# Kernel tuning notes

Measured on AMD Instinct MI355X. Metric: run time of the kernel, lower is better.

The kernel has to match this reference:

```python
import jax, jax.numpy as jnp
import numpy as np

B, P, NB = 16, 10000, 10


def setup_inputs() -> dict:
    key = jax.random.key(0)
    k1, k2, k3, k4 = jax.random.split(key, 4)
    geofeature = jax.random.normal(k1, (B, P, 9), dtype=jnp.float32)
    # neighbor indices into padded T; 0 is the zero-padding row
    nb = jax.random.randint(k2, (P, NB), 0, P + 1)
    reconmatrix = jax.random.normal(k3, (P, P), dtype=jnp.float32) / np.float32(np.sqrt(P))
    vdiff = jax.random.normal(k4, (P, NB, 3), dtype=jnp.float32)
    return {"geofeature": geofeature, "nb": nb, "reconmatrix": reconmatrix, "vdiff": vdiff}


def _ftoT(f):
    # f: [B, P, 9]. First 3 = log-rotation, last 6 = symmetric scale/shear.
    logr = f[..., :3]
    x, y, z = logr[..., 0], logr[..., 1], logr[..., 2]
    theta = jnp.sqrt(jnp.sum(logr * logr, axis=-1))  # [B, P]
    zero = jnp.zeros_like(x)
    # matches torch gather [6,0,1,3,6,2,4,5,6] over [x,y,z,-x,-y,-z,0]:
    # [[0, x, y], [-x, 0, z], [-y, -z, 0]]
    K = jnp.stack([zero, x, y, -x, zero, z, -y, -z, zero], axis=-1)
    K = K.reshape(f.shape[0], f.shape[1], 3, 3)
    cond = theta == 0
    safe_theta = jnp.where(cond, jnp.ones_like(theta), theta)
    Kn = K / safe_theta[..., None, None]
    st = jnp.sin(safe_theta)[..., None, None]
    ct = jnp.cos(safe_theta)[..., None, None]
    I = jnp.eye(3, dtype=f.dtype)
    R_rod = I + Kn * st + jnp.matmul(Kn, Kn) * (1.0 - ct)
    R = jnp.where(cond[..., None, None], I, R_rod)
    # S symmetric from features 3..8 via gather pattern [3,4,5,4,6,7,5,7,8]
    s3, s4, s5, s6, s7, s8 = (f[..., i] for i in range(3, 9))
    S = jnp.stack([s3, s4, s5, s4, s6, s7, s5, s7, s8], axis=-1)
    S = S.reshape(f.shape[0], f.shape[1], 3, 3)
    return jnp.matmul(R, S)  # [B, P, 3, 3]


def reference(geofeature, nb, reconmatrix, vdiff):
    T = _ftoT(geofeature)  # [B, P, 3, 3]
    padded = jnp.concatenate([jnp.zeros((T.shape[0], 1, 3, 3), T.dtype), T], axis=1)
    nb_T = padded[:, nb]                    # [B, P, NB, 3, 3] neighbor gather
    sum_T = nb_T + T[:, :, None]            # [B, P, NB, 3, 3]
    bdiff = jnp.einsum('bpnde,pne->bpnd', sum_T, vdiff)  # [B, P, NB, 3]
    bvec = jnp.sum(bdiff, axis=2)           # [B, P, 3]
    v = jnp.einsum('vp,bpe->bve', reconmatrix, bvec)     # [B, P, 3]
    return v
```

## Files before the change

### kernel.cpp

```cpp
#include <hip/hip_runtime.h>
#include <math.h>

#define B_    16
#define P_    10000
#define NB_   10
#define KBTOT 313
#define KBPAD 328
#define NSMAX 16

typedef __attribute__((ext_vector_type(8))) short bf16x8;
typedef __attribute__((ext_vector_type(4))) float f32x4;

static __device__ __forceinline__ unsigned short f2bf(float f) {
    unsigned u = __float_as_uint(f);
    u += 0x7fffu + ((u >> 16) & 1u);
    return (unsigned short)(u >> 16);
}

__global__ __launch_bounds__(256) void ftoT_kernel(const float* __restrict__ f,
                                                   float* __restrict__ Tm2) {
    int t = blockIdx.x * blockDim.x + threadIdx.x;
    if (t >= B_ * P_) return;
    int p = t >> 4, b = t & 15;
    const float* fp = f + ((size_t)b * P_ + p) * 9;
    float x = fp[0], y = fp[1], z = fp[2];
    float s3 = fp[3], s4 = fp[4], s5 = fp[5], s6 = fp[6], s7 = fp[7], s8 = fp[8];
    float th2 = x * x + y * y + z * z;
    float R00, R01, R02, R10, R11, R12, R20, R21, R22;
    if (th2 == 0.0f) {
        R00 = 1; R01 = 0; R02 = 0; R10 = 0; R11 = 1; R12 = 0; R20 = 0; R21 = 0; R22 = 1;
    } else {
        float theta = sqrtf(th2);
        float inv = 1.0f / theta;
        float kx = x * inv, ky = y * inv, kz = z * inv;
        float st = sinf(theta);
        float omc = 1.0f - cosf(theta);
        R00 = 1.0f - omc * (kx * kx + ky * ky);
        R01 = kx * st - omc * (ky * kz);
        R02 = ky * st + omc * (kx * kz);
        R10 = -kx * st - omc * (ky * kz);
        R11 = 1.0f - omc * (kx * kx + kz * kz);
        R12 = kz * st - omc * (kx * ky);
        R20 = -ky * st + omc * (kx * kz);
        R21 = -kz * st - omc * (kx * ky);
        R22 = 1.0f - omc * (ky * ky + kz * kz);
    }
    float* o = Tm2 + (size_t)t * 12;
    o[0] = R00 * s3 + R01 * s4 + R02 * s5;
    o[1] = R00 * s4 + R01 * s6 + R02 * s7;
    o[2] = R00 * s5 + R01 * s7 + R02 * s8;
    o[3] = R10 * s3 + R11 * s4 + R12 * s5;
    o[4] = R10 * s4 + R11 * s6 + R12 * s7;
    o[5] = R10 * s5 + R11 * s7 + R12 * s8;
    o[6] = R20 * s3 + R21 * s4 + R22 * s5;
    o[7] = R20 * s4 + R21 * s6 + R22 * s7;
    o[8] = R20 * s5 + R21 * s7 + R22 * s8;
    o[9] = 0.0f; o[10] = 0.0f; o[11] = 0.0f;
}

__global__ __launch_bounds__(256) void bvec_kernel(const float* __restrict__ Tm2,
                                                   const int* __restrict__ nb,
                                                   const float* __restrict__ vdiff,
                                                   unsigned short* __restrict__ Bf) {
    int tid = threadIdx.x;
    int bl = tid & 15, pl = tid >> 4;
    int p = blockIdx.x * 16 + pl;
    if (p >= P_) return;

    const float4* Tow = (const float4*)(Tm2 + ((size_t)p * 16 + bl) * 12);
    float4 o0 = Tow[0], o1 = Tow[1], o2 = Tow[2];

    float a0 = 0, a1 = 0, a2 = 0, vs0 = 0, vs1 = 0, vs2 = 0;
#pragma unroll
    for (int n = 0; n < NB_; n++) {
        int idx = nb[p * NB_ + n];
        const float* vd = vdiff + ((size_t)p * NB_ + n) * 3;
        float v0 = vd[0], v1 = vd[1], v2 = vd[2];
        vs0 += v0; vs1 += v1; vs2 += v2;
        if (idx > 0) {
            const float4* Tp = (const float4*)(Tm2 + ((size_t)(idx - 1) * 16 + bl) * 12);
            float4 q0 = Tp[0], q1 = Tp[1], q2 = Tp[2];
            a0 += q0.x * v0 + q0.y * v1 + q0.z * v2;
            a1 += q0.w * v0 + q1.x * v1 + q1.y * v2;
            a2 += q1.z * v0 + q1.w * v1 + q2.x * v2;
        }
    }
    a0 += o0.x * vs0 + o0.y * vs1 + o0.z * vs2;
    a1 += o0.w * vs0 + o1.x * vs1 + o1.y * vs2;
    a2 += o1.z * vs0 + o1.w * vs1 + o2.x * vs2;

    int kb = p >> 5, ii = p & 7, quad = (p >> 3) & 3;
    float vals[3] = {a0, a1, a2};
#pragma unroll
    for (int d = 0; d < 3; d++) {
        int j = bl * 3 + d;
        int t = j >> 4;
        int ln = quad * 16 + (j & 15);
        Bf[(((size_t)kb * 3 + t) * 64 + ln) * 8 + ii] = f2bf(vals[d]);
    }
}

static __device__ __forceinline__ void slot_load(const float* __restrict__ ap,
                                                 const bf16x8* __restrict__ Bv,
                                                 int l, int kb,
                                                 float4& a0, float4& a1,
                                                 bf16x8& b0, bf16x8& b1, bf16x8& b2) {
    const float4* p = (const float4*)(ap + (size_t)kb * 32);
    a0 = p[0]; a1 = p[1];
    size_t bo = (size_t)kb * 192 + l;
    b0 = Bv[bo]; b1 = Bv[bo + 64]; b2 = Bv[bo + 128];
}

static __device__ __forceinline__ void slot_mfma(const float4& a0, const float4& a1,
                                                 const bf16x8& b0, const bf16x8& b1,
                                                 const bf16x8& b2,
                                                 f32x4& acc0, f32x4& acc1, f32x4& acc2) {
    bf16x8 a;
    a[0] = (short)f2bf(a0.x); a[1] = (short)f2bf(a0.y);
    a[2] = (short)f2bf(a0.z); a[3] = (short)f2bf(a0.w);
    a[4] = (short)f2bf(a1.x); a[5] = (short)f2bf(a1.y);
    a[6] = (short)f2bf(a1.z); a[7] = (short)f2bf(a1.w);
    acc0 = __builtin_amdgcn_mfma_f32_16x16x32_bf16(a, b0, acc0, 0, 0, 0);
    acc1 = __builtin_amdgcn_mfma_f32_16x16x32_bf16(a, b1, acc1, 0, 0, 0);
    acc2 = __builtin_amdgcn_mfma_f32_16x16x32_bf16(a, b2, acc2, 0, 0, 0);
}

__global__ __launch_bounds__(256, 4) void gemm_mfma(const float* __restrict__ recon,
                                                    const unsigned short* __restrict__ Bf,
                                                    float* __restrict__ part, int KBC) {
    int l = threadIdx.x & 63;
    int w = threadIdx.x >> 6;
    int r0 = (blockIdx.x * 4 + w) * 16;
    if (r0 >= P_) return;
    int y = blockIdx.y;
    int kb0 = y * KBC;
    int kbend = kb0 + KBC; if (kbend > 320) kbend = 320;
    int kbf = kbend < 312 ? kbend : 312;
    if (kbf < kb0) kbf = kb0;
    int n = l & 15, quad = l >> 4;
    const float* ap = recon + (size_t)(r0 + n) * P_ + quad * 8;
    const bf16x8* Bv = (const bf16x8*)Bf;

    f32x4 acc0 = {0, 0, 0, 0}, acc1 = {0, 0, 0, 0}, acc2 = {0, 0, 0, 0};

    int nfull = kbf - kb0;
    if (nfull >= 2) {
        float4 s0a0, s0a1, s1a0, s1a1;
        bf16x8 s0b0, s0b1, s0b2, s1b0, s1b1, s1b2;
        slot_load(ap, Bv, l, kb0,     s0a0, s0a1, s0b0, s0b1, s0b2);
        slot_load(ap, Bv, l, kb0 + 1, s1a0, s1a1, s1b0, s1b1, s1b2);
        for (int kb = kb0 + 2; kb + 1 < kbf; kb += 2) {
            slot_mfma(s0a0, s0a1, s0b0, s0b1, s0b2, acc0, acc1, acc2);
            slot_load(ap, Bv, l, kb,     s0a0, s0a1, s0b0, s0b1, s0b2);
            slot_mfma(s1a0, s1a1, s1b0, s1b1, s1b2, acc0, acc1, acc2);
            slot_load(ap, Bv, l, kb + 1, s1a0, s1a1, s1b0, s1b1, s1b2);
        }
        slot_mfma(s0a0, s0a1, s0b0, s0b1, s0b2, acc0, acc1, acc2);
        slot_mfma(s1a0, s1a1, s1b0, s1b1, s1b2, acc0, acc1, acc2);
    }

    for (int kb = kbf; kb < kbend; ++kb) {
        int k = kb * 32 + quad * 8;
        bf16x8 a;
        if (k < P_) {
            const float4* apk = (const float4*)(recon + (size_t)(r0 + n) * P_ + k);
            float4 x0 = apk[0], x1 = apk[1];
            a[0] = (short)f2bf(x0.x); a[1] = (short)f2bf(x0.y);
            a[2] = (short)f2bf(x0.z); a[3] = (short)f2bf(x0.w);
            a[4] = (short)f2bf(x1.x); a[5] = (short)f2bf(x1.y);
            a[6] = (short)f2bf(x1.z); a[7] = (short)f2bf(x1.w);
        } else {
            a = (bf16x8)0;
        }
        size_t bo = (size_t)kb * 192 + l;
        bf16x8 b0 = Bv[bo], b1 = Bv[bo + 64], b2 = Bv[bo + 128];
        acc0 = __builtin_amdgcn_mfma_f32_16x16x32_bf16(a, b0, acc0, 0, 0, 0);
        acc1 = __builtin_amdgcn_mfma_f32_16x16x32_bf16(a, b1, acc1, 0, 0, 0);
        acc2 = __builtin_amdgcn_mfma_f32_16x16x32_bf16(a, b2, acc2, 0, 0, 0);
    }

    float* base = part + (size_t)y * (48 * P_);
    int rs = r0 + quad * 4;
    f32x4 accs[3] = {acc0, acc1, acc2};
#pragma unroll
    for (int t = 0; t < 3; t++) {
        int j = t * 16 + n;
        float4 st = make_float4(accs[t][0], accs[t][1], accs[t][2], accs[t][3]);
        *(float4*)(base + (size_t)j * P_ + rs) = st;
    }
}

__global__ __launch_bounds__(256) void reduce_kernel(const float* __restrict__ part,
                                                     float* __restrict__ out, int NS) {
    int i = blockIdx.x * blockDim.x + threadIdx.x;
    if (i >= 48 * P_) return;
    float s = 0.0f;
    for (int z = 0; z < NS; z++) s += part[(size_t)z * (48 * P_) + i];
    int j = i / P_;
    int r = i - j * P_;
    int b = j / 3;
    int d = j - 3 * b;
    out[((size_t)b * P_ + r) * 3 + d] = s;
}

extern "C" void kernel_launch(void* const* d_in, const int* in_sizes, int n_in,
                              void* d_out, int out_size, void* d_ws, size_t ws_size,
                              hipStream_t stream) {
    const float* geo   = (const float*)d_in[0];
    const int*   nb    = (const int*)d_in[1];
    const float* recon = (const float*)d_in[2];
    const float* vdiff = (const float*)d_in[3];
    float* out = (float*)d_out;

    const size_t Tm2F = (size_t)B_ * P_ * 12;
    const size_t BfU  = (size_t)KBPAD * 3 * 64 * 8;
    const size_t BfF  = (BfU + 1) / 2;
    float*          Tm2  = (float*)d_ws;
    unsigned short* Bf   = (unsigned short*)(Tm2 + Tm2F);
    float*          part = Tm2 + Tm2F + BfF;

    size_t ws_floats = ws_size / 4;
    size_t used = Tm2F + BfF;
    size_t avail = (ws_floats > used) ? (ws_floats - used) : 0;
    int NS = (int)(avail / ((size_t)48 * P_));
    if (NS > NSMAX) NS = NSMAX;
    if (NS < 1) NS = 1;
    int KBC = (320 + NS - 1) / NS;
    KBC = (KBC + 3) & ~3;
    int NSeff = (320 + KBC - 1) / KBC;

    hipMemsetAsync(Bf, 0, BfU * sizeof(unsigned short), stream);
    int BP = B_ * P_;
    hipLaunchKernelGGL(ftoT_kernel, dim3((BP + 255) / 256), dim3(256), 0, stream, geo, Tm2);
    hipLaunchKernelGGL(bvec_kernel, dim3((P_ + 15) / 16), dim3(256), 0, stream,
                       Tm2, nb, vdiff, Bf);
    hipLaunchKernelGGL(gemm_mfma, dim3((P_ + 63) / 64, NSeff), dim3(256), 0, stream,
                       recon, Bf, part, KBC);
    hipLaunchKernelGGL(reduce_kernel, dim3((48 * P_ + 255) / 256), dim3(256), 0, stream,
                       part, out, NSeff);
}
```

Baseline: 572.2 us.

## Fuse all stages into one persistent kernel with grid-wide barriers

Replaces the four launches (ftoT, bvec, split-K GEMM, reduce) and the large Bf memset with a single persistent kernel of 628 blocks. The stages are separated by atomic grid barriers, and only the K-padding tail of Bf is zeroed in-kernel. The maximum split-K count drops from 16 to 8. This removes launch gaps and memset traffic, but adds barrier spin cost, needs all blocks to be co-resident, and gives the GEMM less split-K parallelism.

```diff
diff --git a/kernel.cpp b/kernel.cpp
--- a/kernel.cpp
+++ b/kernel.cpp
@@ -1,12 +1,14 @@
 #include <hip/hip_runtime.h>
 #include <math.h>
 
-#define B_    16
-#define P_    10000
-#define NB_   10
-#define KBTOT 313
-#define KBPAD 328
-#define NSMAX 16
+#define B_     16
+#define P_     10000
+#define NB_    10
+#define KBFULL 312
+#define KBLIM  320
+#define NSMAX  8
+#define XTILES 157
+#define GRID_  628
 
 typedef __attribute__((ext_vector_type(8))) short bf16x8;
 typedef __attribute__((ext_vector_type(4))) float f32x4;
@@ -17,87 +19,27 @@
     return (unsigned short)(u >> 16);
 }
 
-__global__ __launch_bounds__(256) void ftoT_kernel(const float* __restrict__ f,
-                                                   float* __restrict__ Tm2) {
-    int t = blockIdx.x * blockDim.x + threadIdx.x;
-    if (t >= B_ * P_) return;
-    int p = t >> 4, b = t & 15;
-    const float* fp = f + ((size_t)b * P_ + p) * 9;
-    float x = fp[0], y = fp[1], z = fp[2];
-    float s3 = fp[3], s4 = fp[4], s5 = fp[5], s6 = fp[6], s7 = fp[7], s8 = fp[8];
-    float th2 = x * x + y * y + z * z;
-    float R00, R01, R02, R10, R11, R12, R20, R21, R22;
-    if (th2 == 0.0f) {
-        R00 = 1; R01 = 0; R02 = 0; R10 = 0; R11 = 1; R12 = 0; R20 = 0; R21 = 0; R22 = 1;
-    } else {
-        float theta = sqrtf(th2);
-        float inv = 1.0f / theta;
-        float kx = x * inv, ky = y * inv, kz = z * inv;
-        float st = sinf(theta);
-        float omc = 1.0f - cosf(theta);
-        R00 = 1.0f - omc * (kx * kx + ky * ky);
-        R01 = kx * st - omc * (ky * kz);
-        R02 = ky * st + omc * (kx * kz);
-        R10 = -kx * st - omc * (ky * kz);
-        R11 = 1.0f - omc * (kx * kx + kz * kz);
-        R12 = kz * st - omc * (kx * ky);
-        R20 = -ky * st + omc * (kx * kz);
-        R21 = -kz * st - omc * (kx * ky);
-        R22 = 1.0f - omc * (ky * ky + kz * kz);
-    }
-    float* o = Tm2 + (size_t)t * 12;
-    o[0] = R00 * s3 + R01 * s4 + R02 * s5;
-    o[1] = R00 * s4 + R01 * s6 + R02 * s7;
-    o[2] = R00 * s5 + R01 * s7 + R02 * s8;
-    o[3] = R10 * s3 + R11 * s4 + R12 * s5;
-    o[4] = R10 * s4 + R11 * s6 + R12 * s7;
-    o[5] = R10 * s5 + R11 * s7 + R12 * s8;
-    o[6] = R20 * s3 + R21 * s4 + R22 * s5;
-    o[7] = R20 * s4 + R21 * s6 + R22 * s7;
-    o[8] = R20 * s5 + R21 * s7 + R22 * s8;
-    o[9] = 0.0f; o[10] = 0.0f; o[11] = 0.0f;
-}
-
-__global__ __launch_bounds__(256) void bvec_kernel(const float* __restrict__ Tm2,
-                                                   const int* __restrict__ nb,
-                                                   const float* __restrict__ vdiff,
-                                                   unsigned short* __restrict__ Bf) {
-    int tid = threadIdx.x;
-    int bl = tid & 15, pl = tid >> 4;
-    int p = blockIdx.x * 16 + pl;
-    if (p >= P_) return;
-
-    const float4* Tow = (const float4*)(Tm2 + ((size_t)p * 16 + bl) * 12);
-    float4 o0 = Tow[0], o1 = Tow[1], o2 = Tow[2];
-
-    float a0 = 0, a1 = 0, a2 = 0, vs0 = 0, vs1 = 0, vs2 = 0;
-#pragma unroll
-    for (int n = 0; n < NB_; n++) {
-        int idx = nb[p * NB_ + n];
-        const float* vd = vdiff + ((size_t)p * NB_ + n) * 3;
-        float v0 = vd[0], v1 = vd[1], v2 = vd[2];
-        vs0 += v0; vs1 += v1; vs2 += v2;
-        if (idx > 0) {
-            const float4* Tp = (const float4*)(Tm2 + ((size_t)(idx - 1) * 16 + bl) * 12);
-            float4 q0 = Tp[0], q1 = Tp[1], q2 = Tp[2];
-            a0 += q0.x * v0 + q0.y * v1 + q0.z * v2;
-            a1 += q0.w * v0 + q1.x * v1 + q1.y * v2;
-            a2 += q1.z * v0 + q1.w * v1 + q2.x * v2;
-        }
-    }
-    a0 += o0.x * vs0 + o0.y * vs1 + o0.z * vs2;
-    a1 += o0.w * vs0 + o1.x * vs1 + o1.y * vs2;
-    a2 += o1.z * vs0 + o1.w * vs1 + o2.x * vs2;
-
-    int kb = p >> 5, ii = p & 7, quad = (p >> 3) & 3;
-    float vals[3] = {a0, a1, a2};
-#pragma unroll
-    for (int d = 0; d < 3; d++) {
-        int j = bl * 3 + d;
-        int t = j >> 4;
-        int ln = quad * 16 + (j & 15);
-        Bf[(((size_t)kb * 3 + t) * 64 + ln) * 8 + ii] = f2bf(vals[d]);
-    }
+static __device__ __forceinline__ void grid_barrier(unsigned* __restrict__ bar,
+                                                    unsigned target_gen) {
+    __syncthreads();
+    if (threadIdx.x == 0) {
+        __threadfence();
+        unsigned prev = __hip_atomic_fetch_add(&bar[0], 1u, __ATOMIC_ACQ_REL,
+                                               __HIP_MEMORY_SCOPE_AGENT);
+        if (prev == (unsigned)GRID_ - 1u) {
+            __hip_atomic_store(&bar[0], 0u, __ATOMIC_RELAXED, __HIP_MEMORY_SCOPE_AGENT);
+            __hip_atomic_store(&bar[16], target_gen, __ATOMIC_RELEASE,
+                               __HIP_MEMORY_SCOPE_AGENT);
+        } else {
+            unsigned g;
+            do {
+                g = __hip_atomic_load(&bar[16], __ATOMIC_ACQUIRE, __HIP_MEMORY_SCOPE_AGENT);
+                if (g < target_gen) __builtin_amdgcn_s_sleep(2);
+            } while (g < target_gen);
+        }
+        __threadfence();
+    }
+    __syncthreads();
 }
 
 static __device__ __forceinline__ void slot_load(const float* __restrict__ ap,
@@ -125,117 +67,209 @@
     acc2 = __builtin_amdgcn_mfma_f32_16x16x32_bf16(a, b2, acc2, 0, 0, 0);
 }
 
-__global__ __launch_bounds__(256, 4) void gemm_mfma(const float* __restrict__ recon,
-                                                    const unsigned short* __restrict__ Bf,
-                                                    float* __restrict__ part, int KBC) {
-    int l = threadIdx.x & 63;
-    int w = threadIdx.x >> 6;
-    int r0 = (blockIdx.x * 4 + w) * 16;
-    if (r0 >= P_) return;
-    int y = blockIdx.y;
-    int kb0 = y * KBC;
-    int kbend = kb0 + KBC; if (kbend > 320) kbend = 320;
-    int kbf = kbend < 312 ? kbend : 312;
-    if (kbf < kb0) kbf = kb0;
-    int n = l & 15, quad = l >> 4;
-    const float* ap = recon + (size_t)(r0 + n) * P_ + quad * 8;
-    const bf16x8* Bv = (const bf16x8*)Bf;
-
-    f32x4 acc0 = {0, 0, 0, 0}, acc1 = {0, 0, 0, 0}, acc2 = {0, 0, 0, 0};
-
-    int nfull = kbf - kb0;
-    if (nfull >= 2) {
-        float4 s0a0, s0a1, s1a0, s1a1;
-        bf16x8 s0b0, s0b1, s0b2, s1b0, s1b1, s1b2;
-        slot_load(ap, Bv, l, kb0,     s0a0, s0a1, s0b0, s0b1, s0b2);
-        slot_load(ap, Bv, l, kb0 + 1, s1a0, s1a1, s1b0, s1b1, s1b2);
-        for (int kb = kb0 + 2; kb + 1 < kbf; kb += 2) {
-            slot_mfma(s0a0, s0a1, s0b0, s0b1, s0b2, acc0, acc1, acc2);
-            slot_load(ap, Bv, l, kb,     s0a0, s0a1, s0b0, s0b1, s0b2);
-            slot_mfma(s1a0, s1a1, s1b0, s1b1, s1b2, acc0, acc1, acc2);
-            slot_load(ap, Bv, l, kb + 1, s1a0, s1a1, s1b0, s1b1, s1b2);
-        }
-        slot_mfma(s0a0, s0a1, s0b0, s0b1, s0b2, acc0, acc1, acc2);
-        slot_mfma(s1a0, s1a1, s1b0, s1b1, s1b2, acc0, acc1, acc2);
-    }
-
-    for (int kb = kbf; kb < kbend; ++kb) {
-        int k = kb * 32 + quad * 8;
-        bf16x8 a;
-        if (k < P_) {
-            const float4* apk = (const float4*)(recon + (size_t)(r0 + n) * P_ + k);
-            float4 x0 = apk[0], x1 = apk[1];
-            a[0] = (short)f2bf(x0.x); a[1] = (short)f2bf(x0.y);
-            a[2] = (short)f2bf(x0.z); a[3] = (short)f2bf(x0.w);
-            a[4] = (short)f2bf(x1.x); a[5] = (short)f2bf(x1.y);
-            a[6] = (short)f2bf(x1.z); a[7] = (short)f2bf(x1.w);
+__global__ __launch_bounds__(256, 4) void fused_all(
+    const float* __restrict__ geo, const int* __restrict__ nbid,
+    const float* __restrict__ recon, const float* __restrict__ vdiff,
+    float* __restrict__ out, float* __restrict__ Tm2,
+    unsigned short* __restrict__ Bf, float* __restrict__ part,
+    unsigned* __restrict__ bar, int NS, int KBC)
+{
+    const int tid  = threadIdx.x;
+    const int gtid = blockIdx.x * blockDim.x + tid;
+    const int gstr = GRID_ * 256;
+
+    for (int t = gtid; t < B_ * P_; t += gstr) {
+        int p = t >> 4, b = t & 15;
+        const float* fp = geo + ((size_t)b * P_ + p) * 9;
+        float x = fp[0], y = fp[1], z = fp[2];
+        float s3 = fp[3], s4 = fp[4], s5 = fp[5], s6 = fp[6], s7 = fp[7], s8 = fp[8];
+        float th2 = x * x + y * y + z * z;
+        float R00, R01, R02, R10, R11, R12, R20, R21, R22;
+        if (th2 == 0.0f) {
+            R00 = 1; R01 = 0; R02 = 0; R10 = 0; R11 = 1; R12 = 0; R20 = 0; R21 = 0; R22 = 1;
         } else {
-            a = (bf16x8)0;
-        }
-        size_t bo = (size_t)kb * 192 + l;
-        bf16x8 b0 = Bv[bo], b1 = Bv[bo + 64], b2 = Bv[bo + 128];
-        acc0 = __builtin_amdgcn_mfma_f32_16x16x32_bf16(a, b0, acc0, 0, 0, 0);
-        acc1 = __builtin_amdgcn_mfma_f32_16x16x32_bf16(a, b1, acc1, 0, 0, 0);
-        acc2 = __builtin_amdgcn_mfma_f32_16x16x32_bf16(a, b2, acc2, 0, 0, 0);
-    }
-
-    float* base = part + (size_t)y * (48 * P_);
-    int rs = r0 + quad * 4;
-    f32x4 accs[3] = {acc0, acc1, acc2};
+            float theta = sqrtf(th2);
+            float inv = 1.0f / theta;
+            float kx = x * inv, ky = y * inv, kz = z * inv;
+            float st = sinf(theta);
+            float omc = 1.0f - cosf(theta);
+            R00 = 1.0f - omc * (kx * kx + ky * ky);
+            R01 = kx * st - omc * (ky * kz);
+            R02 = ky * st + omc * (kx * kz);
+            R10 = -kx * st - omc * (ky * kz);
+            R11 = 1.0f - omc * (kx * kx + kz * kz);
+            R12 = kz * st - omc * (kx * ky);
+            R20 = -ky * st + omc * (kx * kz);
+            R21 = -kz * st - omc * (kx * ky);
+            R22 = 1.0f - omc * (ky * ky + kz * kz);
+        }
+        float* o = Tm2 + (size_t)t * 12;
+        o[0] = R00 * s3 + R01 * s4 + R02 * s5;
+        o[1] = R00 * s4 + R01 * s6 + R02 * s7;
+        o[2] = R00 * s5 + R01 * s7 + R02 * s8;
+        o[3] = R10 * s3 + R11 * s4 + R12 * s5;
+        o[4] = R10 * s4 + R11 * s6 + R12 * s7;
+        o[5] = R10 * s5 + R11 * s7 + R12 * s8;
+        o[6] = R20 * s3 + R21 * s4 + R22 * s5;
+        o[7] = R20 * s4 + R21 * s6 + R22 * s7;
+        o[8] = R20 * s5 + R21 * s7 + R22 * s8;
+        o[9] = 0.0f; o[10] = 0.0f; o[11] = 0.0f;
+    }
+    {
+        unsigned int* bz = (unsigned int*)(Bf + (size_t)KBFULL * 1536);
+        for (int i = gtid; i < (KBLIM - KBFULL) * 768; i += gstr) bz[i] = 0u;
+    }
+    grid_barrier(bar, 1u);
+
+    {
+        int bl = tid & 15, pl = tid >> 4;
+        for (int bi = blockIdx.x; bi < (P_ + 15) / 16; bi += GRID_) {
+            int p = bi * 16 + pl;
+            if (p < P_) {
+                const float4* Tow = (const float4*)(Tm2 + ((size_t)p * 16 + bl) * 12);
+                float4 o0 = Tow[0], o1 = Tow[1], o2 = Tow[2];
+
+                float a0 = 0, a1 = 0, a2 = 0, vs0 = 0, vs1 = 0, vs2 = 0;
 #pragma unroll
-    for (int t = 0; t < 3; t++) {
-        int j = t * 16 + n;
-        float4 st = make_float4(accs[t][0], accs[t][1], accs[t][2], accs[t][3]);
-        *(float4*)(base + (size_t)j * P_ + rs) = st;
-    }
-}
-
-__global__ __launch_bounds__(256) void reduce_kernel(const float* __restrict__ part,
-                                                     float* __restrict__ out, int NS) {
-    int i = blockIdx.x * blockDim.x + threadIdx.x;
-    if (i >= 48 * P_) return;
-    float s = 0.0f;
-    for (int z = 0; z < NS; z++) s += part[(size_t)z * (48 * P_) + i];
-    int j = i / P_;
-    int r = i - j * P_;
-    int b = j / 3;
-    int d = j - 3 * b;
-    out[((size_t)b * P_ + r) * 3 + d] = s;
+                for (int n = 0; n < NB_; n++) {
+                    int idx = nbid[p * NB_ + n];
+                    const float* vd = vdiff + ((size_t)p * NB_ + n) * 3;
+                    float v0 = vd[0], v1 = vd[1], v2 = vd[2];
+                    vs0 += v0; vs1 += v1; vs2 += v2;
+                    if (idx > 0) {
+                        const float4* Tp = (const float4*)(Tm2 + ((size_t)(idx - 1) * 16 + bl) * 12);
+                        float4 q0 = Tp[0], q1 = Tp[1], q2 = Tp[2];
+                        a0 += q0.x * v0 + q0.y * v1 + q0.z * v2;
+                        a1 += q0.w * v0 + q1.x * v1 + q1.y * v2;
+                        a2 += q1.z * v0 + q1.w * v1 + q2.x * v2;
+                    }
+                }
+                a0 += o0.x * vs0 + o0.y * vs1 + o0.z * vs2;
+                a1 += o0.w * vs0 + o1.x * vs1 + o1.y * vs2;
+                a2 += o1.z * vs0 + o1.w * vs1 + o2.x * vs2;
+
+                int kb = p >> 5, ii = p & 7, quad = (p >> 3) & 3;
+                float vals[3] = {a0, a1, a2};
+#pragma unroll
+                for (int d = 0; d < 3; d++) {
+                    int j = bl * 3 + d;
+                    int t = j >> 4;
+                    int ln = quad * 16 + (j & 15);
+                    Bf[(((size_t)kb * 3 + t) * 64 + ln) * 8 + ii] = f2bf(vals[d]);
+                }
+            }
+        }
+    }
+    grid_barrier(bar, 2u);
+
+    {
+        int l = tid & 63, w = tid >> 6;
+        int n = l & 15, quad = l >> 4;
+        const bf16x8* Bv = (const bf16x8*)Bf;
+        int NU = XTILES * NS;
+        for (int u = blockIdx.x; u < NU; u += GRID_) {
+            int y = u / XTILES;
+            int x = u - y * XTILES;
+            int r0 = (x * 4 + w) * 16;
+            if (r0 < P_) {
+                int kb0 = y * KBC;
+                int kbend = kb0 + KBC; if (kbend > KBLIM) kbend = KBLIM;
+                int kbf = kbend < KBFULL ? kbend : KBFULL;
+                if (kbf < kb0) kbf = kb0;
+                const float* ap = recon + (size_t)(r0 + n) * P_ + quad * 8;
+
+                f32x4 acc0 = {0, 0, 0, 0}, acc1 = {0, 0, 0, 0}, acc2 = {0, 0, 0, 0};
+
+                int nfull = kbf - kb0;
+                if (nfull >= 2) {
+                    float4 s0a0, s0a1, s1a0, s1a1;
+                    bf16x8 s0b0, s0b1, s0b2, s1b0, s1b1, s1b2;
+                    slot_load(ap, Bv, l, kb0,     s0a0, s0a1, s0b0, s0b1, s0b2);
+                    slot_load(ap, Bv, l, kb0 + 1, s1a0, s1a1, s1b0, s1b1, s1b2);
+                    for (int kb = kb0 + 2; kb + 1 < kbf; kb += 2) {
+                        slot_mfma(s0a0, s0a1, s0b0, s0b1, s0b2, acc0, acc1, acc2);
+                        slot_load(ap, Bv, l, kb,     s0a0, s0a1, s0b0, s0b1, s0b2);
+                        slot_mfma(s1a0, s1a1, s1b0, s1b1, s1b2, acc0, acc1, acc2);
+                        slot_load(ap, Bv, l, kb + 1, s1a0, s1a1, s1b0, s1b1, s1b2);
+                    }
+                    slot_mfma(s0a0, s0a1, s0b0, s0b1, s0b2, acc0, acc1, acc2);
+                    slot_mfma(s1a0, s1a1, s1b0, s1b1, s1b2, acc0, acc1, acc2);
+                }
+
+                for (int kb = kbf; kb < kbend; ++kb) {
+                    int k = kb * 32 + quad * 8;
+                    bf16x8 a;
+                    if (k < P_) {
+                        const float4* apk = (const float4*)(recon + (size_t)(r0 + n) * P_ + k);
+                        float4 x0 = apk[0], x1 = apk[1];
+                        a[0] = (short)f2bf(x0.x); a[1] = (short)f2bf(x0.y);
+                        a[2] = (short)f2bf(x0.z); a[3] = (short)f2bf(x0.w);
+                        a[4] = (short)f2bf(x1.x); a[5] = (short)f2bf(x1.y);
+                        a[6] = (short)f2bf(x1.z); a[7] = (short)f2bf(x1.w);
+                    } else {
+                        a = (bf16x8)0;
+                    }
+                    size_t bo = (size_t)kb * 192 + l;
+                    bf16x8 b0 = Bv[bo], b1 = Bv[bo + 64], b2 = Bv[bo + 128];
+                    acc0 = __builtin_amdgcn_mfma_f32_16x16x32_bf16(a, b0, acc0, 0, 0, 0);
+                    acc1 = __builtin_amdgcn_mfma_f32_16x16x32_bf16(a, b1, acc1, 0, 0, 0);
+                    acc2 = __builtin_amdgcn_mfma_f32_16x16x32_bf16(a, b2, acc2, 0, 0, 0);
+                }
+
+                float* base = part + (size_t)y * (48 * P_);
+                int rs = r0 + quad * 4;
+                f32x4 accs[3] = {acc0, acc1, acc2};
+#pragma unroll
+                for (int t = 0; t < 3; t++) {
+                    int j = t * 16 + n;
+                    float4 st = make_float4(accs[t][0], accs[t][1], accs[t][2], accs[t][3]);
+                    *(float4*)(base + (size_t)j * P_ + rs) = st;
+                }
+            }
+        }
+    }
+    grid_barrier(bar, 3u);
+
+    for (int i = gtid; i < 48 * P_; i += gstr) {
+        float s = 0.0f;
+        for (int z = 0; z < NS; z++) s += part[(size_t)z * (48 * P_) + i];
+        int j = i / P_;
+        int r = i - j * P_;
+        int b = j / 3;
+        int d = j - 3 * b;
+        out[((size_t)b * P_ + r) * 3 + d] = s;
+    }
 }
 
 extern "C" void kernel_launch(void* const* d_in, const int* in_sizes, int n_in,
                               void* d_out, int out_size, void* d_ws, size_t ws_size,
                               hipStream_t stream) {
     const float* geo   = (const float*)d_in[0];
-    const int*   nb    = (const int*)d_in[1];
+    const int*   nbid  = (const int*)d_in[1];
     const float* recon = (const float*)d_in[2];
     const float* vdiff = (const float*)d_in[3];
     float* out = (float*)d_out;
 
     const size_t Tm2F = (size_t)B_ * P_ * 12;
-    const size_t BfU  = (size_t)KBPAD * 3 * 64 * 8;
+    const size_t BfU  = (size_t)KBLIM * 3 * 64 * 8;
     const size_t BfF  = (BfU + 1) / 2;
+    const size_t BarF = 64;
     float*          Tm2  = (float*)d_ws;
     unsigned short* Bf   = (unsigned short*)(Tm2 + Tm2F);
-    float*          part = Tm2 + Tm2F + BfF;
+    unsigned*       bar  = (unsigned*)(Tm2 + Tm2F + BfF);
+    float*          part = Tm2 + Tm2F + BfF + BarF;
 
     size_t ws_floats = ws_size / 4;
-    size_t used = Tm2F + BfF;
+    size_t used = Tm2F + BfF + BarF;
     size_t avail = (ws_floats > used) ? (ws_floats - used) : 0;
     int NS = (int)(avail / ((size_t)48 * P_));
     if (NS > NSMAX) NS = NSMAX;
     if (NS < 1) NS = 1;
-    int KBC = (320 + NS - 1) / NS;
+    int KBC = (KBLIM + NS - 1) / NS;
     KBC = (KBC + 3) & ~3;
-    int NSeff = (320 + KBC - 1) / KBC;
-
-    hipMemsetAsync(Bf, 0, BfU * sizeof(unsigned short), stream);
-    int BP = B_ * P_;
-    hipLaunchKernelGGL(ftoT_kernel, dim3((BP + 255) / 256), dim3(256), 0, stream, geo, Tm2);
-    hipLaunchKernelGGL(bvec_kernel, dim3((P_ + 15) / 16), dim3(256), 0, stream,
-                       Tm2, nb, vdiff, Bf);
-    hipLaunchKernelGGL(gemm_mfma, dim3((P_ + 63) / 64, NSeff), dim3(256), 0, stream,
-                       recon, Bf, part, KBC);
-    hipLaunchKernelGGL(reduce_kernel, dim3((48 * P_ + 255) / 256), dim3(256), 0, stream,
-                       part, out, NSeff);
-}
+    int NSeff = (KBLIM + KBC - 1) / KBC;
+
+    hipMemsetAsync(bar, 0, BarF * sizeof(float), stream);
+    hipLaunchKernelGGL(fused_all, dim3(GRID_), dim3(256), 0, stream,
+                       geo, nbid, recon, vdiff, out, Tm2, Bf, part, bar, NSeff, KBC);
+}
```

Result: slower. 1.227 ms (+114.5%).
